# Optimization experiments

Measured on AMD Instinct MI355X. Metric: run time of the kernel, lower is better.

## Reference

```python
import jax, jax.numpy as jnp
import numpy as np
import math

DT = 1.0
BETA = 15.0
TAU0 = 3.0
THRESHOLD = 0.25


def setup_inputs() -> dict:
    key = jax.random.key(0)
    B, F, L = 64, 256, 2048
    I = jax.random.normal(key, (B, F, L), dtype=jnp.float32)
    raw0 = math.log(math.expm1(TAU0))
    raw_tau = jnp.full((F,), raw0, dtype=jnp.float32)
    thr = jnp.float32(THRESHOLD)
    return {"I": I, "raw_tau": raw_tau, "thr": thr}


def reference(I, raw_tau, thr):
    B, F, L = I.shape
    tau = jax.nn.softplus(raw_tau) + 1e-4          # [F]
    alpha = jnp.exp(-DT / tau).astype(I.dtype)      # [F] decay per filter

    def step(v, I_t):
        # v: [B, F], I_t: [B, F]
        v_pre = alpha * v + (1.0 - alpha) * I_t
        z = BETA * (v_pre - thr)
        s = (v_pre >= thr).astype(I.dtype)
        v_new = v_pre * (1.0 - s)                   # hard reset on spike
        return v_new, (z, s)

    I_time = jnp.moveaxis(I, -1, 0)                 # [L, B, F]
    v0 = jnp.zeros((B, F), dtype=I.dtype)
    _, (z_hist, s_hist) = jax.lax.scan(step, v0, I_time)
    # back to [B, F, L]
    return jnp.moveaxis(z_hist, 0, -1), jnp.moveaxis(s_hist, 0, -1)
```

## Files before the change

### kernel.cpp

```cpp
#include <hip/hip_runtime.h>
#include <cmath>

#define LIF_L 2048
#define LIF_F 256
#define LIF_B 64
#define LIF_BF (LIF_B * LIF_F)

__global__ __launch_bounds__(64) void lif_scan_kernel(
    const float* __restrict__ I, const float* __restrict__ raw_tau,
    const float* __restrict__ thr_p, float* __restrict__ out) {
#pragma clang fp contract(off)
  const int chain = blockIdx.x * 64 + threadIdx.x;
  const int f = chain & (LIF_F - 1);

  const double rt = (double)raw_tau[f];
  const double splus = (rt > 0.0) ? (rt + log1p(exp(-rt))) : log1p(exp(rt));
  const float alpha = (float)exp(-1.0 / (splus + 1e-4));
  const float oma = 1.0f - alpha;
  const float thr = thr_p[0];
  const float beta = 15.0f;

  const float4* __restrict__ Ip = (const float4*)(I + (size_t)chain * LIF_L);
  float4* __restrict__ Zp = (float4*)(out + (size_t)chain * LIF_L);
  float4* __restrict__ Sp =
      (float4*)(out + (size_t)LIF_BF * LIF_L + (size_t)chain * LIF_L);

  float v = 0.0f;
  float4 buf[2][4];
#pragma unroll
  for (int j = 0; j < 4; ++j) buf[0][j] = Ip[j];

  const int NCH = LIF_L / 16;
  for (int c = 0; c < NCH; ++c) {
    const int cur = c & 1;
    if (c + 1 < NCH) {
#pragma unroll
      for (int j = 0; j < 4; ++j) buf[cur ^ 1][j] = Ip[(c + 1) * 4 + j];
    }
#pragma unroll
    for (int j = 0; j < 4; ++j) {
      const float4 in = buf[cur][j];
      float4 z, s;
      float vpre;

      vpre = alpha * v + oma * in.x;
      s.x = (vpre >= thr) ? 1.0f : 0.0f;
      z.x = beta * (vpre - thr);
      v = (vpre >= thr) ? 0.0f : vpre;

      vpre = alpha * v + oma * in.y;
      s.y = (vpre >= thr) ? 1.0f : 0.0f;
      z.y = beta * (vpre - thr);
      v = (vpre >= thr) ? 0.0f : vpre;

      vpre = alpha * v + oma * in.z;
      s.z = (vpre >= thr) ? 1.0f : 0.0f;
      z.z = beta * (vpre - thr);
      v = (vpre >= thr) ? 0.0f : vpre;

      vpre = alpha * v + oma * in.w;
      s.w = (vpre >= thr) ? 1.0f : 0.0f;
      z.w = beta * (vpre - thr);
      v = (vpre >= thr) ? 0.0f : vpre;

      Zp[c * 4 + j] = z;
      Sp[c * 4 + j] = s;
    }
  }
}

extern "C" void kernel_launch(void* const* d_in, const int* in_sizes, int n_in,
                              void* d_out, int out_size, void* d_ws,
                              size_t ws_size, hipStream_t stream) {
  const float* I = (const float*)d_in[0];
  const float* raw_tau = (const float*)d_in[1];
  const float* thr = (const float*)d_in[2];
  float* out = (float*)d_out;
  dim3 grid(LIF_BF / 64), block(64);
  lif_scan_kernel<<<grid, block, 0, stream>>>(I, raw_tau, thr, out);
}
```

Baseline: 470.5 us.

## Stage time tiles through LDS for coalesced loads and stores

Each wave now loads 64x64 time tiles cooperatively, so groups of 16 lanes read contiguous 256-byte row segments into padded LDS. Each lane then runs its sequential scan over its own LDS row and writes z/s back through LDS for coalesced float4 stores. Before, each lane streamed its own 8KB row with float4 accesses 8KB apart, giving uncoalesced traffic. The cost is extra LDS traffic, more LDS per block (about 50KB, which limits occupancy), and scalar LDS accesses inside the serial loop.

```diff
diff --git a/kernel.cpp b/kernel.cpp
--- a/kernel.cpp
+++ b/kernel.cpp
@@ -5,67 +5,84 @@
 #define LIF_F 256
 #define LIF_B 64
 #define LIF_BF (LIF_B * LIF_F)
+#define TT 64
+#define NTILE (LIF_L / TT)
+#define STR 65
 
 __global__ __launch_bounds__(64) void lif_scan_kernel(
     const float* __restrict__ I, const float* __restrict__ raw_tau,
     const float* __restrict__ thr_p, float* __restrict__ out) {
 #pragma clang fp contract(off)
-  const int chain = blockIdx.x * 64 + threadIdx.x;
-  const int f = chain & (LIF_F - 1);
+  __shared__ float ldsI[64 * STR];
+  __shared__ float ldsZ[64 * STR];
+  __shared__ float ldsS[64 * STR];
 
+  const int lane = threadIdx.x;
+  const int cbase = blockIdx.x * 64;
+  const int q = lane >> 4;
+  const int m = lane & 15;
+
+  const int f = (cbase + lane) & (LIF_F - 1);
   const double rt = (double)raw_tau[f];
-  const double splus = (rt > 0.0) ? (rt + log1p(exp(-rt))) : log1p(exp(rt));
-  const float alpha = (float)exp(-1.0 / (splus + 1e-4));
+  const double sp = (rt > 0.0) ? (rt + log1p(exp(-rt))) : log1p(exp(rt));
+  const float alpha = (float)exp(-1.0 / (sp + 1e-4));
   const float oma = 1.0f - alpha;
   const float thr = thr_p[0];
   const float beta = 15.0f;
 
-  const float4* __restrict__ Ip = (const float4*)(I + (size_t)chain * LIF_L);
-  float4* __restrict__ Zp = (float4*)(out + (size_t)chain * LIF_L);
-  float4* __restrict__ Sp =
-      (float4*)(out + (size_t)LIF_BF * LIF_L + (size_t)chain * LIF_L);
+  const float4* __restrict__ Ip = (const float4*)I;
+  float4* __restrict__ Zp = (float4*)out;
+  float4* __restrict__ Sp = (float4*)(out + (size_t)LIF_BF * LIF_L);
 
   float v = 0.0f;
-  float4 buf[2][4];
+  float4 inbuf[16];
+
 #pragma unroll
-  for (int j = 0; j < 4; ++j) buf[0][j] = Ip[j];
+  for (int k = 0; k < 16; ++k) {
+    const int row = 4 * k + q;
+    inbuf[k] = Ip[(size_t)(cbase + row) * (LIF_L / 4) + m];
+  }
 
-  const int NCH = LIF_L / 16;
-  for (int c = 0; c < NCH; ++c) {
-    const int cur = c & 1;
-    if (c + 1 < NCH) {
+  for (int tile = 0; tile < NTILE; ++tile) {
 #pragma unroll
-      for (int j = 0; j < 4; ++j) buf[cur ^ 1][j] = Ip[(c + 1) * 4 + j];
+    for (int k = 0; k < 16; ++k) {
+      const int row = 4 * k + q;
+      float* p = &ldsI[row * STR + 4 * m];
+      p[0] = inbuf[k].x; p[1] = inbuf[k].y; p[2] = inbuf[k].z; p[3] = inbuf[k].w;
     }
+    const int tn = (tile + 1 < NTILE) ? tile + 1 : tile;
 #pragma unroll
-    for (int j = 0; j < 4; ++j) {
-      const float4 in = buf[cur][j];
-      float4 z, s;
-      float vpre;
+    for (int k = 0; k < 16; ++k) {
+      const int row = 4 * k + q;
+      inbuf[k] = Ip[(size_t)(cbase + row) * (LIF_L / 4) + tn * (TT / 4) + m];
+    }
+    __builtin_amdgcn_wave_barrier();
 
-      vpre = alpha * v + oma * in.x;
-      s.x = (vpre >= thr) ? 1.0f : 0.0f;
-      z.x = beta * (vpre - thr);
+    float* rowI = &ldsI[lane * STR];
+    float* rowZ = &ldsZ[lane * STR];
+    float* rowS = &ldsS[lane * STR];
+#pragma unroll 8
+    for (int t = 0; t < TT; ++t) {
+      const float in = rowI[t];
+      const float vpre = alpha * v + oma * in;
+      rowZ[t] = beta * (vpre - thr);
+      rowS[t] = (vpre >= thr) ? 1.0f : 0.0f;
       v = (vpre >= thr) ? 0.0f : vpre;
+    }
+    __builtin_amdgcn_wave_barrier();
 
-      vpre = alpha * v + oma * in.y;
-      s.y = (vpre >= thr) ? 1.0f : 0.0f;
-      z.y = beta * (vpre - thr);
-      v = (vpre >= thr) ? 0.0f : vpre;
-
-      vpre = alpha * v + oma * in.z;
-      s.z = (vpre >= thr) ? 1.0f : 0.0f;
-      z.z = beta * (vpre - thr);
-      v = (vpre >= thr) ? 0.0f : vpre;
-
-      vpre = alpha * v + oma * in.w;
-      s.w = (vpre >= thr) ? 1.0f : 0.0f;
-      z.w = beta * (vpre - thr);
-      v = (vpre >= thr) ? 0.0f : vpre;
-
-      Zp[c * 4 + j] = z;
-      Sp[c * 4 + j] = s;
+#pragma unroll
+    for (int k = 0; k < 16; ++k) {
+      const int row = 4 * k + q;
+      const size_t oidx = (size_t)(cbase + row) * (LIF_L / 4) + tile * (TT / 4) + m;
+      const float* pz = &ldsZ[row * STR + 4 * m];
+      float4 zv = {pz[0], pz[1], pz[2], pz[3]};
+      Zp[oidx] = zv;
+      const float* ps = &ldsS[row * STR + 4 * m];
+      float4 sv = {ps[0], ps[1], ps[2], ps[3]};
+      Sp[oidx] = sv;
     }
+    __builtin_amdgcn_wave_barrier();
   }
 }
 
```

Result: faster. 386.1 us (-17.9%).
